# Kernel tuning notes

Measured on AMD Instinct MI355X. Metric: run time of the kernel, lower is better.

Reference implementation:

```python
import jax, jax.numpy as jnp
import numpy as np

HIDDEN = 128
CHNLS = 21
B = 2
T = 15000


def conv1d(x, w, b, stride, pad, groups):
    # x: [N, Cin, L], w: [Cout, Cin/groups, K]
    y = jax.lax.conv_general_dilated(
        x, w, window_strides=(stride,), padding=[(pad, pad)],
        feature_group_count=groups, dimension_numbers=('NCH', 'OIH', 'NCH'))
    return y + b[None, :, None]


def setup_inputs() -> dict:
    key = jax.random.key(0)
    ks = jax.random.split(key, 12)
    d = {}
    d['x'] = jax.random.normal(ks[0], (B, T, CHNLS), dtype=jnp.float32)
    d['ch_vector'] = jax.random.randint(ks[1], (B, CHNLS), 0, CHNLS)
    outs = [HIDDEN // 16 * CHNLS, HIDDEN // 8 * CHNLS, HIDDEN // 4 * CHNLS,
            HIDDEN // 2 * CHNLS, HIDDEN * CHNLS]
    kers = [7, 7, 7, 7, 9]
    for i in range(5):
        d[f'w{i+1}'] = jax.random.normal(ks[2 + i], (outs[i], 1, kers[i]), dtype=jnp.float32) * 0.1
        d[f'b{i+1}'] = jnp.zeros((outs[i],), dtype=jnp.float32)
    d['ch_table'] = jax.random.normal(ks[7], (CHNLS, 512), dtype=jnp.float32) * 0.05
    for i in range(4):
        d[f'mw{i+1}'] = jax.random.normal(ks[8 + i], (1, 1, 4), dtype=jnp.float32) * 0.3
        d[f'mb{i+1}'] = jnp.zeros((1,), dtype=jnp.float32)
    return d


def reference(x, ch_vector, w1, b1, w2, b2, w3, b3, w4, b4, w5, b5,
              ch_table, mw1, mb1, mw2, mb2, mw3, mb3, mw4, mb4):
    # ---- depthwise-style grouped conv stack (groups == in_channels) ----
    h = jnp.transpose(x, (0, 2, 1))                    # [B, CHNLS, T]
    h = conv1d(h, w1, b1, 2, 0, h.shape[1])
    h = conv1d(h, w2, b2, 2, 0, h.shape[1])
    h = conv1d(h, w3, b3, 2, 0, h.shape[1])
    h = conv1d(h, w4, b4, 2, 0, h.shape[1])
    h = conv1d(h, w5, b5, 2, 0, h.shape[1])            # [B, HIDDEN*CHNLS, Tr]

    emb = jnp.transpose(h, (0, 2, 1))                  # [B, Tr, HIDDEN*CHNLS]
    Tr = emb.shape[1]
    emb = emb.reshape(B, Tr, HIDDEN, CHNLS)            # matches torch reshape

    ch_emb = ch_table[ch_vector]                       # [B, CHNLS, 512]
    # torch.einsum('abik, adkj -> abij') with d == 1
    w = jnp.einsum('btik,bkj->btij', emb, ch_emb)      # [B, Tr, HIDDEN, 512]
    w = w.reshape(B, Tr, HIDDEN * 512)

    # ---- per-timestep 1->1 conv stack, batched over B*Tr instead of a loop ----
    z = w.reshape(B * Tr, 1, HIDDEN * 512)
    z = conv1d(z, mw1, mb1, 2, 1, 1)
    z = conv1d(z, mw2, mb2, 2, 1, 1)
    z = jax.nn.gelu(z, approximate=False)
    z = conv1d(z, mw3, mb3, 2, 1, 1)
    z = conv1d(z, mw4, mb4, 2, 1, 1)
    z = jax.nn.gelu(z, approximate=False)              # [B*Tr, 1, HIDDEN*32]
    return z.reshape(B, Tr, HIDDEN * 32)
```

## Files before the change

kernel.cpp:

```cpp
#include <hip/hip_runtime.h>
#include <math.h>


#define NB 2
#define TR 462
#define C5 2688
#define OUTROW 4096

#define T5  42
#define L0T 1531
#define L1T 763
#define L2T 379
#define L3T 187
#define L4T 91
#define SS1 768
#define SS2 384
#define SS3 192
#define SS4 93

__device__ __forceinline__ float gelu_exact(float x) {
    return 0.5f * x * (1.0f + erff(x * 0.7071067811865476f));
}

__device__ __forceinline__ int swz(int a) { return a ^ (((a >> 7) & 7) << 2); }

__device__ __forceinline__ void composite10(const float* A, const float* Bv, float* c) {
#pragma unroll
    for (int r = 0; r < 10; ++r) {
        float acc = 0.f;
#pragma unroll
        for (int p = 0; p < 4; ++p) {
            int q = r - 2 * p;
            if (q >= 0 && q < 4) acc = fmaf(A[p], Bv[q], acc);
        }
        c[r] = acc;
    }
}

__global__ __launch_bounds__(512)
void conv_stack_prep_kernel(const float* __restrict__ x,
                            const float* __restrict__ w1, const float* __restrict__ b1,
                            const float* __restrict__ w2, const float* __restrict__ b2,
                            const float* __restrict__ w3, const float* __restrict__ b3,
                            const float* __restrict__ w4, const float* __restrict__ b4,
                            const float* __restrict__ w5, const float* __restrict__ b5,
                            const float* __restrict__ table, const int* __restrict__ chv,
                            const float* __restrict__ mw1, const float* __restrict__ mw2,
                            float* __restrict__ embT,
                            float* __restrict__ cheCT, float* __restrict__ cheLN4)
{
    const int tile = blockIdx.x;
    const int c    = blockIdx.y;
    const int b    = blockIdx.z;
    const int tid  = threadIdx.x;

    if (tile == 11) {
        if (c != 0 || tid >= 128) return;
        const int m = tid;
        float W1[4], W2[4], c2[10];
#pragma unroll
        for (int q = 0; q < 4; ++q) { W1[q] = mw1[q]; W2[q] = mw2[q]; }
        composite10(W2, W1, c2);
        for (int k = 0; k < 21; ++k) {
            const float* cb = table + (long)chv[b * 21 + k] * 512;
            float acc = 0.f;
            if (m == 0) {
#pragma unroll
                for (int r = 3; r < 10; ++r) acc = fmaf(c2[r], cb[r - 3], acc);
            } else if (m == 127) {
#pragma unroll
                for (int r = 0; r < 7; ++r) acc = fmaf(c2[r], cb[505 + r], acc);
            } else {
                int j0 = 4 * m - 3;
#pragma unroll
                for (int r = 0; r < 10; ++r) acc = fmaf(c2[r], cb[j0 + r], acc);
            }
            cheCT[b * 2688 + m * 21 + k] = acc;
        }
        if (m < 21) {
            const float* cb = table + (long)chv[b * 21 + m] * 512;
            float l = 0.f, n = 0.f;
#pragma unroll
            for (int r = 0; r < 3; ++r)  l = fmaf(c2[r], cb[509 + r], l);
#pragma unroll
            for (int r = 7; r < 10; ++r) n = fmaf(c2[r], cb[r - 7], n);
            cheLN4[b * 84 + m]      = l;
            cheLN4[b * 84 + 21 + m] = n;
            cheLN4[b * 84 + 42 + m] = cb[0];
            cheLN4[b * 84 + 63 + m] = cb[511];
        }
        return;
    }

    __shared__ __align__(16) float A[6144];
    __shared__ __align__(16) float B[6144];
    const int lane = tid & 63;
    const int wq   = tid >> 6;
    const int t0   = tile * T5;

    {
        const float* xp = x + (long)b * 315000L + (long)(32 * t0) * 21L + c;
        for (int i = tid; i < L0T; i += 512) A[i] = xp[(long)i * 21L];
    }
    __syncthreads();

    auto convK7 = [&](const float* SIN, int sstride, bool from_x,
                      float* SOUT, int ostride,
                      const float* wg, const float* bg, int wbase,
                      int nch, int pairs, int Lout, bool b64st) {
        for (int it = 0; it < (nch >> 3); ++it) {
            const int chg = __builtin_amdgcn_readfirstlane((it << 3) + wq);
            const float* wp = wg + (size_t)(wbase + chg) * 7;
            const float W0 = wp[0], Wa = wp[1], Wb = wp[2], Wc = wp[3],
                        Wd = wp[4], We = wp[5], Wf = wp[6];
            const float bb = bg[wbase + chg];
            const float* sin_ch = SIN + (from_x ? 0 : (chg >> 1) * sstride);
            float* sout_ch = SOUT + chg * ostride;
            for (int j = lane; j < pairs; j += 64) {
                const int p = 2 * j;
                const float* s = sin_ch + p * 2;
                const float4 u0 = *(const float4*)(s);
                const float4 u1 = *(const float4*)(s + 4);
                const float4 u2 = *(const float4*)(s + 8);
                float o0 = bb, o1 = bb;
                o0 = fmaf(W0, u0.x, o0); o0 = fmaf(Wa, u0.y, o0); o0 = fmaf(Wb, u0.z, o0);
                o0 = fmaf(Wc, u0.w, o0); o0 = fmaf(Wd, u1.x, o0); o0 = fmaf(We, u1.y, o0);
                o0 = fmaf(Wf, u1.z, o0);
                o1 = fmaf(W0, u0.z, o1); o1 = fmaf(Wa, u0.w, o1); o1 = fmaf(Wb, u1.x, o1);
                o1 = fmaf(Wc, u1.y, o1); o1 = fmaf(Wd, u1.z, o1); o1 = fmaf(We, u1.w, o1);
                o1 = fmaf(Wf, u2.x, o1);
                if (p + 1 < Lout) {
                    if (b64st) *(float2*)(sout_ch + p) = make_float2(o0, o1);
                    else       { sout_ch[p] = o0; sout_ch[p + 1] = o1; }
                } else {
                    sout_ch[p] = o0;
                }
            }
        }
    };

    convK7(A, 0,   true,  B, SS1, w1, b1, 8 * c,  8,  382, L1T, true);
    __syncthreads();
    convK7(B, SS1, false, A, SS2, w2, b2, 16 * c, 16, 190, L2T, true);
    __syncthreads();
    convK7(A, SS2, false, B, SS3, w3, b3, 32 * c, 32, 94,  L3T, true);
    __syncthreads();
    convK7(B, SS3, false, A, SS4, w4, b4, 64 * c, 64, 46,  L4T, false);
    __syncthreads();

    {
        const int ch5 = tid & 127;
        const int th  = tid >> 7;
        const float* wp = w5 + (size_t)(128 * c + ch5) * 9;
        float V[9];
#pragma unroll
        for (int k = 0; k < 9; ++k) V[k] = wp[k];
        const float bb = b5[128 * c + ch5];
        const float* s4ch = A + (ch5 >> 1) * SS4;
        float* obase = embT + ((long)(b * TR + t0)) * C5 + 128 * c + ch5;
#pragma unroll
        for (int iu = 0; iu < 11; ++iu) {
            const int tl = th + 4 * iu;
            if (tl < T5) {
                const float* sp = s4ch + 2 * tl;
                float acc = bb;
#pragma unroll
                for (int k = 0; k < 9; ++k) acc = fmaf(V[k], sp[k], acc);
                obase[(long)tl * C5] = acc;
            }
        }
    }
}

__global__ __launch_bounds__(1024)
void fused_embed_kernel(const float* __restrict__ embT,
                        const float* __restrict__ cheCT,
                        const float* __restrict__ cheLN4,
                        const float* __restrict__ mw1, const float* __restrict__ mb1,
                        const float* __restrict__ mw2, const float* __restrict__ mb2,
                        const float* __restrict__ mw3, const float* __restrict__ mb3,
                        const float* __restrict__ mw4, const float* __restrict__ mb4,
                        float* __restrict__ out)
{
    __shared__ float s_g2[16400];
    __shared__ float s_emb[2688];
    __shared__ float s_ln[84];

    const int t   = blockIdx.x;
    const int b   = blockIdx.y;
    const int tid = threadIdx.x;
    const int i   = tid & 127;
    const int mq  = __builtin_amdgcn_readfirstlane(tid >> 7);

    const float* erow = embT + ((long)(b * TR + t)) * C5;
    if (tid < 672) *(float4*)&s_emb[tid * 4] = ((const float4*)erow)[tid];
    if (tid >= 672 && tid < 756) s_ln[tid - 672] = cheLN4[b * 84 + (tid - 672)];
    if (tid >= 768 && tid < 772)       s_g2[tid - 768] = 0.f;
    else if (tid >= 772 && tid < 788)  s_g2[16380 + (tid - 772) + 4] = 0.f;

    float W1[4], W2[4], W3[4], W4[4];
#pragma unroll
    for (int q = 0; q < 4; ++q) { W1[q] = mw1[q]; W2[q] = mw2[q]; W3[q] = mw3[q]; W4[q] = mw4[q]; }
    const float B1 = mb1[0], B2 = mb2[0], B3 = mb3[0], B4 = mb4[0];
    const float Bc = B2 + B1 * (W2[0] + W2[1] + W2[2] + W2[3]);

    __syncthreads();

    float er[21];
#pragma unroll
    for (int k = 0; k < 21; ++k) er[k] = s_emb[i * 21 + k];

    const float* cp = cheCT + (b * 128 + mq * 16) * 21;
#pragma unroll
    for (int mi4 = 0; mi4 < 4; ++mi4) {
        const int m0 = mq * 16 + mi4 * 4;
        const float* cc = cp + mi4 * 84;
        float z0 = Bc, z1 = Bc, z2 = Bc, z3 = Bc;
#pragma unroll
        for (int k = 0; k < 21; ++k) {
            const float e = er[k];
            z0 = fmaf(e, cc[k],      z0);
            z1 = fmaf(e, cc[21 + k], z1);
            z2 = fmaf(e, cc[42 + k], z2);
            z3 = fmaf(e, cc[63 + k], z3);
        }
        if (mi4 == 0 && mq == 0) {
            float corr = 0.f;
            if (i == 0) {
                float w0 = 0.f;
#pragma unroll
                for (int k = 0; k < 21; ++k) w0 = fmaf(er[k], s_ln[42 + k], w0);
                corr = -W2[0] * (B1 + W1[3] * w0);
            } else {
#pragma unroll
                for (int k = 0; k < 21; ++k) corr = fmaf(s_emb[(i - 1) * 21 + k], s_ln[k], corr);
            }
            z0 += corr;
        }
        if (mi4 == 3 && mq == 7) {
            float corr = 0.f;
            if (i == 127) {
                float wl = 0.f;
#pragma unroll
                for (int k = 0; k < 21; ++k) wl = fmaf(er[k], s_ln[63 + k], wl);
                corr = -W2[3] * (B1 + W1[0] * wl);
            } else {
#pragma unroll
                for (int k = 0; k < 21; ++k) corr = fmaf(s_emb[(i + 1) * 21 + k], s_ln[21 + k], corr);
            }
            z3 += corr;
        }
        float4 q;
        q.x = gelu_exact(z0);
        q.y = gelu_exact(z1);
        q.z = gelu_exact(z2);
        q.w = gelu_exact(z3);
        *(float4*)&s_g2[swz(4 + i * 128 + m0)] = q;
    }
    __syncthreads();

    float c4[10];
    composite10(W4, W3, c4);
    const float Bc2 = B4 + B3 * (W4[0] + W4[1] + W4[2] + W4[3]);
    float* orow = out + ((long)(b * TR + t)) * OUTROW;
#pragma unroll
    for (int s = 0; s < 4; ++s) {
        const int p  = tid + 1024 * s;
        const int a0 = 4 * p;
        const float4 v0 = *(const float4*)&s_g2[swz(a0)];
        const float4 v1 = *(const float4*)&s_g2[swz(a0 + 4)];
        const float4 v2 = *(const float4*)&s_g2[swz(a0 + 8)];
        const float buf[12] = { v0.x, v0.y, v0.z, v0.w,
                                v1.x, v1.y, v1.z, v1.w,
                                v2.x, v2.y, v2.z, v2.w };
        float z = Bc2;
#pragma unroll
        for (int r = 0; r < 10; ++r) z = fmaf(c4[r], buf[r + 1], z);
        if (p == 0)    z -= W4[0] * (B3 + W3[3] * s_g2[swz(4)]);
        if (p == 4095) z -= W4[3] * (B3 + W3[0] * s_g2[swz(16387)]);
        orow[p] = gelu_exact(z);
    }
}

extern "C" void kernel_launch(void* const* d_in, const int* in_sizes, int n_in,
                              void* d_out, int out_size, void* d_ws, size_t ws_size,
                              hipStream_t stream)
{
    const float* x   = (const float*)d_in[0];
    const int*   chv = (const int*)d_in[1];
    const float* w1  = (const float*)d_in[2];  const float* b1 = (const float*)d_in[3];
    const float* w2  = (const float*)d_in[4];  const float* b2 = (const float*)d_in[5];
    const float* w3  = (const float*)d_in[6];  const float* b3 = (const float*)d_in[7];
    const float* w4  = (const float*)d_in[8];  const float* b4 = (const float*)d_in[9];
    const float* w5  = (const float*)d_in[10]; const float* b5 = (const float*)d_in[11];
    const float* tab = (const float*)d_in[12];
    const float* mw1 = (const float*)d_in[13]; const float* mb1 = (const float*)d_in[14];
    const float* mw2 = (const float*)d_in[15]; const float* mb2 = (const float*)d_in[16];
    const float* mw3 = (const float*)d_in[17]; const float* mb3 = (const float*)d_in[18];
    const float* mw4 = (const float*)d_in[19]; const float* mb4 = (const float*)d_in[20];
    float* outp = (float*)d_out;

    float* ws     = (float*)d_ws;
    float* embT   = ws;
    float* cheCT  = ws + 2483712;
    float* cheLN4 = ws + 2489088;

    {
        dim3 grid(12, 21, NB);
        conv_stack_prep_kernel<<<grid, 512, 0, stream>>>(x, w1, b1, w2, b2, w3, b3,
                                                         w4, b4, w5, b5,
                                                         tab, chv, mw1, mw2,
                                                         embT, cheCT, cheLN4);
    }
    {
        dim3 grid(TR, NB);
        fused_embed_kernel<<<grid, 1024, 0, stream>>>(embT, cheCT, cheLN4,
                                                      mw1, mb1, mw2, mb2, mw3, mb3, mw4, mb4,
                                                      outp);
    }
}
```

Measured before the change: 49.44 us.

## Merge conv stack and embed kernels into one cooperative persistent kernel

```diff
diff --git a/kernel.cpp b/kernel.cpp
--- a/kernel.cpp
+++ b/kernel.cpp
@@ -1,11 +1,15 @@
 #include <hip/hip_runtime.h>
+#include <hip/hip_cooperative_groups.h>
 #include <math.h>
+
+namespace cg = cooperative_groups;
 
 
 #define NB 2
 #define TR 462
 #define C5 2688
 #define OUTROW 4096
+#define GRIDB 256
 
 #define T5  42
 #define L0T 1531
@@ -37,248 +41,253 @@
     }
 }
 
-__global__ __launch_bounds__(512)
-void conv_stack_prep_kernel(const float* __restrict__ x,
-                            const float* __restrict__ w1, const float* __restrict__ b1,
-                            const float* __restrict__ w2, const float* __restrict__ b2,
-                            const float* __restrict__ w3, const float* __restrict__ b3,
-                            const float* __restrict__ w4, const float* __restrict__ b4,
-                            const float* __restrict__ w5, const float* __restrict__ b5,
-                            const float* __restrict__ table, const int* __restrict__ chv,
-                            const float* __restrict__ mw1, const float* __restrict__ mw2,
-                            float* __restrict__ embT,
-                            float* __restrict__ cheCT, float* __restrict__ cheLN4)
+__global__ __launch_bounds__(1024, 1)
+void mono_kernel(const float* __restrict__ x,
+                 const float* __restrict__ w1, const float* __restrict__ b1,
+                 const float* __restrict__ w2, const float* __restrict__ b2,
+                 const float* __restrict__ w3, const float* __restrict__ b3,
+                 const float* __restrict__ w4, const float* __restrict__ b4,
+                 const float* __restrict__ w5, const float* __restrict__ b5,
+                 const float* __restrict__ table, const int* __restrict__ chv,
+                 const float* __restrict__ mw1, const float* __restrict__ mb1,
+                 const float* __restrict__ mw2, const float* __restrict__ mb2,
+                 const float* __restrict__ mw3, const float* __restrict__ mb3,
+                 const float* __restrict__ mw4, const float* __restrict__ mb4,
+                 float* __restrict__ embT, float* __restrict__ cheCT,
+                 float* __restrict__ cheLN4, float* __restrict__ out)
 {
-    const int tile = blockIdx.x;
-    const int c    = blockIdx.y;
-    const int b    = blockIdx.z;
-    const int tid  = threadIdx.x;
-
-    if (tile == 11) {
-        if (c != 0 || tid >= 128) return;
-        const int m = tid;
-        float W1[4], W2[4], c2[10];
-#pragma unroll
-        for (int q = 0; q < 4; ++q) { W1[q] = mw1[q]; W2[q] = mw2[q]; }
-        composite10(W2, W1, c2);
-        for (int k = 0; k < 21; ++k) {
-            const float* cb = table + (long)chv[b * 21 + k] * 512;
-            float acc = 0.f;
-            if (m == 0) {
-#pragma unroll
-                for (int r = 3; r < 10; ++r) acc = fmaf(c2[r], cb[r - 3], acc);
-            } else if (m == 127) {
-#pragma unroll
-                for (int r = 0; r < 7; ++r) acc = fmaf(c2[r], cb[505 + r], acc);
-            } else {
-                int j0 = 4 * m - 3;
-#pragma unroll
-                for (int r = 0; r < 10; ++r) acc = fmaf(c2[r], cb[j0 + r], acc);
-            }
-            cheCT[b * 2688 + m * 21 + k] = acc;
-        }
-        if (m < 21) {
-            const float* cb = table + (long)chv[b * 21 + m] * 512;
-            float l = 0.f, n = 0.f;
-#pragma unroll
-            for (int r = 0; r < 3; ++r)  l = fmaf(c2[r], cb[509 + r], l);
-#pragma unroll
-            for (int r = 7; r < 10; ++r) n = fmaf(c2[r], cb[r - 7], n);
-            cheLN4[b * 84 + m]      = l;
-            cheLN4[b * 84 + 21 + m] = n;
-            cheLN4[b * 84 + 42 + m] = cb[0];
-            cheLN4[b * 84 + 63 + m] = cb[511];
-        }
-        return;
-    }
-
-    __shared__ __align__(16) float A[6144];
-    __shared__ __align__(16) float B[6144];
-    const int lane = tid & 63;
-    const int wq   = tid >> 6;
-    const int t0   = tile * T5;
+    __shared__ __align__(16) float smem[24744];
+
+    const int bk  = blockIdx.x;
+    const int tid = threadIdx.x;
 
     {
-        const float* xp = x + (long)b * 315000L + (long)(32 * t0) * 21L + c;
-        for (int i = tid; i < L0T; i += 512) A[i] = xp[(long)i * 21L];
-    }
-    __syncthreads();
-
-    auto convK7 = [&](const float* SIN, int sstride, bool from_x,
-                      float* SOUT, int ostride,
-                      const float* wg, const float* bg, int wbase,
-                      int nch, int pairs, int Lout, bool b64st) {
-        for (int it = 0; it < (nch >> 3); ++it) {
-            const int chg = __builtin_amdgcn_readfirstlane((it << 3) + wq);
-            const float* wp = wg + (size_t)(wbase + chg) * 7;
-            const float W0 = wp[0], Wa = wp[1], Wb = wp[2], Wc = wp[3],
-                        Wd = wp[4], We = wp[5], Wf = wp[6];
-            const float bb = bg[wbase + chg];
-            const float* sin_ch = SIN + (from_x ? 0 : (chg >> 1) * sstride);
-            float* sout_ch = SOUT + chg * ostride;
-            for (int j = lane; j < pairs; j += 64) {
-                const int p = 2 * j;
-                const float* s = sin_ch + p * 2;
-                const float4 u0 = *(const float4*)(s);
-                const float4 u1 = *(const float4*)(s + 4);
-                const float4 u2 = *(const float4*)(s + 8);
-                float o0 = bb, o1 = bb;
-                o0 = fmaf(W0, u0.x, o0); o0 = fmaf(Wa, u0.y, o0); o0 = fmaf(Wb, u0.z, o0);
-                o0 = fmaf(Wc, u0.w, o0); o0 = fmaf(Wd, u1.x, o0); o0 = fmaf(We, u1.y, o0);
-                o0 = fmaf(Wf, u1.z, o0);
-                o1 = fmaf(W0, u0.z, o1); o1 = fmaf(Wa, u0.w, o1); o1 = fmaf(Wb, u1.x, o1);
-                o1 = fmaf(Wc, u1.y, o1); o1 = fmaf(Wd, u1.z, o1); o1 = fmaf(We, u1.w, o1);
-                o1 = fmaf(Wf, u2.x, o1);
-                if (p + 1 < Lout) {
-                    if (b64st) *(float2*)(sout_ch + p) = make_float2(o0, o1);
-                    else       { sout_ch[p] = o0; sout_ch[p + 1] = o1; }
+        const int h   = tid >> 9;
+        const int tl  = tid & 511;
+        const int job = 2 * bk + h;
+        if (job < 462) {
+            const int tile = job % 11;
+            const int c    = (job / 11) % 21;
+            const int b    = job / 231;
+            float* A = smem + h * 12288;
+            float* B = A + 6144;
+            const int lane = tl & 63;
+            const int wq   = tl >> 6;
+            const int t0   = tile * T5;
+
+            const float* xp = x + (long)b * 315000L + (long)(32 * t0) * 21L + c;
+            for (int i2 = tl; i2 < L0T; i2 += 512) A[i2] = xp[(long)i2 * 21L];
+            __syncthreads();
+
+            auto convK7 = [&](const float* SIN, int sstride, bool from_x,
+                              float* SOUT, int ostride,
+                              const float* wg, const float* bg, int wbase,
+                              int nch, int pairs, int Lout, bool b64st) {
+                for (int it = 0; it < (nch >> 3); ++it) {
+                    const int chg = __builtin_amdgcn_readfirstlane((it << 3) + wq);
+                    const float* wp = wg + (size_t)(wbase + chg) * 7;
+                    const float W0 = wp[0], Wa = wp[1], Wb = wp[2], Wc = wp[3],
+                                Wd = wp[4], We = wp[5], Wf = wp[6];
+                    const float bb = bg[wbase + chg];
+                    const float* sin_ch = SIN + (from_x ? 0 : (chg >> 1) * sstride);
+                    float* sout_ch = SOUT + chg * ostride;
+                    for (int j = lane; j < pairs; j += 64) {
+                        const int p = 2 * j;
+                        const float* s = sin_ch + p * 2;
+                        const float4 u0 = *(const float4*)(s);
+                        const float4 u1 = *(const float4*)(s + 4);
+                        const float4 u2 = *(const float4*)(s + 8);
+                        float o0 = bb, o1 = bb;
+                        o0 = fmaf(W0, u0.x, o0); o0 = fmaf(Wa, u0.y, o0); o0 = fmaf(Wb, u0.z, o0);
+                        o0 = fmaf(Wc, u0.w, o0); o0 = fmaf(Wd, u1.x, o0); o0 = fmaf(We, u1.y, o0);
+                        o0 = fmaf(Wf, u1.z, o0);
+                        o1 = fmaf(W0, u0.z, o1); o1 = fmaf(Wa, u0.w, o1); o1 = fmaf(Wb, u1.x, o1);
+                        o1 = fmaf(Wc, u1.y, o1); o1 = fmaf(Wd, u1.z, o1); o1 = fmaf(We, u1.w, o1);
+                        o1 = fmaf(Wf, u2.x, o1);
+                        if (p + 1 < Lout) {
+                            if (b64st) *(float2*)(sout_ch + p) = make_float2(o0, o1);
+                            else       { sout_ch[p] = o0; sout_ch[p + 1] = o1; }
+                        } else {
+                            sout_ch[p] = o0;
+                        }
+                    }
+                }
+            };
+
+            convK7(A, 0,   true,  B, SS1, w1, b1, 8 * c,  8,  382, L1T, true);
+            __syncthreads();
+            convK7(B, SS1, false, A, SS2, w2, b2, 16 * c, 16, 190, L2T, true);
+            __syncthreads();
+            convK7(A, SS2, false, B, SS3, w3, b3, 32 * c, 32, 94,  L3T, true);
+            __syncthreads();
+            convK7(B, SS3, false, A, SS4, w4, b4, 64 * c, 64, 46,  L4T, false);
+            __syncthreads();
+
+            {
+                const int ch5 = tl & 127;
+                const int th  = (tl >> 7) & 3;
+                const float* wp = w5 + (size_t)(128 * c + ch5) * 9;
+                float V[9];
+#pragma unroll
+                for (int k = 0; k < 9; ++k) V[k] = wp[k];
+                const float bb = b5[128 * c + ch5];
+                const float* s4ch = A + (ch5 >> 1) * SS4;
+                float* obase = embT + ((long)(b * TR + t0)) * C5 + 128 * c + ch5;
+#pragma unroll
+                for (int iu = 0; iu < 11; ++iu) {
+                    const int tl5 = th + 4 * iu;
+                    if (tl5 < T5) {
+                        const float* sp = s4ch + 2 * tl5;
+                        float acc = bb;
+#pragma unroll
+                        for (int k = 0; k < 9; ++k) acc = fmaf(V[k], sp[k], acc);
+                        obase[(long)tl5 * C5] = acc;
+                    }
+                }
+            }
+        } else if (job < 464 && tl < 128) {
+            const int b = job - 462;
+            const int m = tl;
+            float W1[4], W2[4], c2[10];
+#pragma unroll
+            for (int q = 0; q < 4; ++q) { W1[q] = mw1[q]; W2[q] = mw2[q]; }
+            composite10(W2, W1, c2);
+            for (int k = 0; k < 21; ++k) {
+                const float* cb = table + (long)chv[b * 21 + k] * 512;
+                float acc = 0.f;
+                if (m == 0) {
+#pragma unroll
+                    for (int r = 3; r < 10; ++r) acc = fmaf(c2[r], cb[r - 3], acc);
+                } else if (m == 127) {
+#pragma unroll
+                    for (int r = 0; r < 7; ++r) acc = fmaf(c2[r], cb[505 + r], acc);
                 } else {
-                    sout_ch[p] = o0;
-                }
-            }
-        }
-    };
-
-    convK7(A, 0,   true,  B, SS1, w1, b1, 8 * c,  8,  382, L1T, true);
-    __syncthreads();
-    convK7(B, SS1, false, A, SS2, w2, b2, 16 * c, 16, 190, L2T, true);
-    __syncthreads();
-    convK7(A, SS2, false, B, SS3, w3, b3, 32 * c, 32, 94,  L3T, true);
-    __syncthreads();
-    convK7(B, SS3, false, A, SS4, w4, b4, 64 * c, 64, 46,  L4T, false);
-    __syncthreads();
-
-    {
-        const int ch5 = tid & 127;
-        const int th  = tid >> 7;
-        const float* wp = w5 + (size_t)(128 * c + ch5) * 9;
-        float V[9];
-#pragma unroll
-        for (int k = 0; k < 9; ++k) V[k] = wp[k];
-        const float bb = b5[128 * c + ch5];
-        const float* s4ch = A + (ch5 >> 1) * SS4;
-        float* obase = embT + ((long)(b * TR + t0)) * C5 + 128 * c + ch5;
-#pragma unroll
-        for (int iu = 0; iu < 11; ++iu) {
-            const int tl = th + 4 * iu;
-            if (tl < T5) {
-                const float* sp = s4ch + 2 * tl;
-                float acc = bb;
-#pragma unroll
-                for (int k = 0; k < 9; ++k) acc = fmaf(V[k], sp[k], acc);
-                obase[(long)tl * C5] = acc;
+                    int j0 = 4 * m - 3;
+#pragma unroll
+                    for (int r = 0; r < 10; ++r) acc = fmaf(c2[r], cb[j0 + r], acc);
+                }
+                cheCT[b * 2688 + m * 21 + k] = acc;
+            }
+            if (m < 21) {
+                const float* cb = table + (long)chv[b * 21 + m] * 512;
+                float l = 0.f, n = 0.f;
+#pragma unroll
+                for (int r = 0; r < 3; ++r)  l = fmaf(c2[r], cb[509 + r], l);
+#pragma unroll
+                for (int r = 7; r < 10; ++r) n = fmaf(c2[r], cb[r - 7], n);
+                cheLN4[b * 84 + m]      = l;
+                cheLN4[b * 84 + 21 + m] = n;
+                cheLN4[b * 84 + 42 + m] = cb[0];
+                cheLN4[b * 84 + 63 + m] = cb[511];
             }
         }
     }
-}
-
-__global__ __launch_bounds__(1024)
-void fused_embed_kernel(const float* __restrict__ embT,
-                        const float* __restrict__ cheCT,
-                        const float* __restrict__ cheLN4,
-                        const float* __restrict__ mw1, const float* __restrict__ mb1,
-                        const float* __restrict__ mw2, const float* __restrict__ mb2,
-                        const float* __restrict__ mw3, const float* __restrict__ mb3,
-                        const float* __restrict__ mw4, const float* __restrict__ mb4,
-                        float* __restrict__ out)
-{
-    __shared__ float s_g2[16400];
-    __shared__ float s_emb[2688];
-    __shared__ float s_ln[84];
-
-    const int t   = blockIdx.x;
-    const int b   = blockIdx.y;
-    const int tid = threadIdx.x;
-    const int i   = tid & 127;
-    const int mq  = __builtin_amdgcn_readfirstlane(tid >> 7);
-
-    const float* erow = embT + ((long)(b * TR + t)) * C5;
-    if (tid < 672) *(float4*)&s_emb[tid * 4] = ((const float4*)erow)[tid];
-    if (tid >= 672 && tid < 756) s_ln[tid - 672] = cheLN4[b * 84 + (tid - 672)];
-    if (tid >= 768 && tid < 772)       s_g2[tid - 768] = 0.f;
-    else if (tid >= 772 && tid < 788)  s_g2[16380 + (tid - 772) + 4] = 0.f;
+
+    cg::this_grid().sync();
+
+    float* s_g2  = smem;
+    float* s_emb = smem + 16400;
+    float* s_ln  = smem + 24576;
+
+    if (tid < 168) s_ln[tid] = cheLN4[tid];
+    if (tid >= 256 && tid < 260) s_g2[tid - 256] = 0.f;
+    if (tid >= 260 && tid < 276) s_g2[16384 + (tid - 260)] = 0.f;
 
     float W1[4], W2[4], W3[4], W4[4];
 #pragma unroll
     for (int q = 0; q < 4; ++q) { W1[q] = mw1[q]; W2[q] = mw2[q]; W3[q] = mw3[q]; W4[q] = mw4[q]; }
     const float B1 = mb1[0], B2 = mb2[0], B3 = mb3[0], B4 = mb4[0];
     const float Bc = B2 + B1 * (W2[0] + W2[1] + W2[2] + W2[3]);
-
-    __syncthreads();
-
-    float er[21];
-#pragma unroll
-    for (int k = 0; k < 21; ++k) er[k] = s_emb[i * 21 + k];
-
-    const float* cp = cheCT + (b * 128 + mq * 16) * 21;
-#pragma unroll
-    for (int mi4 = 0; mi4 < 4; ++mi4) {
-        const int m0 = mq * 16 + mi4 * 4;
-        const float* cc = cp + mi4 * 84;
-        float z0 = Bc, z1 = Bc, z2 = Bc, z3 = Bc;
-#pragma unroll
-        for (int k = 0; k < 21; ++k) {
-            const float e = er[k];
-            z0 = fmaf(e, cc[k],      z0);
-            z1 = fmaf(e, cc[21 + k], z1);
-            z2 = fmaf(e, cc[42 + k], z2);
-            z3 = fmaf(e, cc[63 + k], z3);
-        }
-        if (mi4 == 0 && mq == 0) {
-            float corr = 0.f;
-            if (i == 0) {
-                float w0 = 0.f;
-#pragma unroll
-                for (int k = 0; k < 21; ++k) w0 = fmaf(er[k], s_ln[42 + k], w0);
-                corr = -W2[0] * (B1 + W1[3] * w0);
-            } else {
-#pragma unroll
-                for (int k = 0; k < 21; ++k) corr = fmaf(s_emb[(i - 1) * 21 + k], s_ln[k], corr);
-            }
-            z0 += corr;
-        }
-        if (mi4 == 3 && mq == 7) {
-            float corr = 0.f;
-            if (i == 127) {
-                float wl = 0.f;
-#pragma unroll
-                for (int k = 0; k < 21; ++k) wl = fmaf(er[k], s_ln[63 + k], wl);
-                corr = -W2[3] * (B1 + W1[0] * wl);
-            } else {
-#pragma unroll
-                for (int k = 0; k < 21; ++k) corr = fmaf(s_emb[(i + 1) * 21 + k], s_ln[21 + k], corr);
-            }
-            z3 += corr;
-        }
-        float4 q;
-        q.x = gelu_exact(z0);
-        q.y = gelu_exact(z1);
-        q.z = gelu_exact(z2);
-        q.w = gelu_exact(z3);
-        *(float4*)&s_g2[swz(4 + i * 128 + m0)] = q;
-    }
-    __syncthreads();
-
     float c4[10];
     composite10(W4, W3, c4);
     const float Bc2 = B4 + B3 * (W4[0] + W4[1] + W4[2] + W4[3]);
-    float* orow = out + ((long)(b * TR + t)) * OUTROW;
-#pragma unroll
-    for (int s = 0; s < 4; ++s) {
-        const int p  = tid + 1024 * s;
-        const int a0 = 4 * p;
-        const float4 v0 = *(const float4*)&s_g2[swz(a0)];
-        const float4 v1 = *(const float4*)&s_g2[swz(a0 + 4)];
-        const float4 v2 = *(const float4*)&s_g2[swz(a0 + 8)];
-        const float buf[12] = { v0.x, v0.y, v0.z, v0.w,
-                                v1.x, v1.y, v1.z, v1.w,
-                                v2.x, v2.y, v2.z, v2.w };
-        float z = Bc2;
-#pragma unroll
-        for (int r = 0; r < 10; ++r) z = fmaf(c4[r], buf[r + 1], z);
-        if (p == 0)    z -= W4[0] * (B3 + W3[3] * s_g2[swz(4)]);
-        if (p == 4095) z -= W4[3] * (B3 + W3[0] * s_g2[swz(16387)]);
-        orow[p] = gelu_exact(z);
+
+    const int i  = tid & 127;
+    const int mq = __builtin_amdgcn_readfirstlane(tid >> 7);
+
+    for (int r = 0; r < 4; ++r) {
+        const int job = bk + 256 * r;
+        if (job < NB * TR) {
+            const int t = job % TR;
+            const int b = job / TR;
+            const float* lnb = s_ln + b * 84;
+
+            const float* erow = embT + ((long)(b * TR + t)) * C5;
+            if (tid < 672) *(float4*)&s_emb[tid * 4] = ((const float4*)erow)[tid];
+            __syncthreads();
+
+            float er[21];
+#pragma unroll
+            for (int k = 0; k < 21; ++k) er[k] = s_emb[i * 21 + k];
+
+            const float* cp = cheCT + (b * 128 + mq * 16) * 21;
+#pragma unroll
+            for (int mi4 = 0; mi4 < 4; ++mi4) {
+                const int m0 = mq * 16 + mi4 * 4;
+                const float* cc = cp + mi4 * 84;
+                float z0 = Bc, z1 = Bc, z2 = Bc, z3 = Bc;
+#pragma unroll
+                for (int k = 0; k < 21; ++k) {
+                    const float e = er[k];
+                    z0 = fmaf(e, cc[k],      z0);
+                    z1 = fmaf(e, cc[21 + k], z1);
+                    z2 = fmaf(e, cc[42 + k], z2);
+                    z3 = fmaf(e, cc[63 + k], z3);
+                }
+                if (mi4 == 0 && mq == 0) {
+                    float corr = 0.f;
+                    if (i == 0) {
+                        float w0 = 0.f;
+#pragma unroll
+                        for (int k = 0; k < 21; ++k) w0 = fmaf(er[k], lnb[42 + k], w0);
+                        corr = -W2[0] * (B1 + W1[3] * w0);
+                    } else {
+#pragma unroll
+                        for (int k = 0; k < 21; ++k) corr = fmaf(s_emb[(i - 1) * 21 + k], lnb[k], corr);
+                    }
+                    z0 += corr;
+                }
+                if (mi4 == 3 && mq == 7) {
+                    float corr = 0.f;
+                    if (i == 127) {
+                        float wl = 0.f;
+#pragma unroll
+                        for (int k = 0; k < 21; ++k) wl = fmaf(er[k], lnb[63 + k], wl);
+                        corr = -W2[3] * (B1 + W1[0] * wl);
+                    } else {
+#pragma unroll
+                        for (int k = 0; k < 21; ++k) corr = fmaf(s_emb[(i + 1) * 21 + k], lnb[21 + k], corr);
+                    }
+                    z3 += corr;
+                }
+                float4 q;
+                q.x = gelu_exact(z0);
+                q.y = gelu_exact(z1);
+                q.z = gelu_exact(z2);
+                q.w = gelu_exact(z3);
+                *(float4*)&s_g2[swz(4 + i * 128 + m0)] = q;
+            }
+            __syncthreads();
+
+            float* orow = out + ((long)(b * TR + t)) * OUTROW;
+#pragma unroll
+            for (int s = 0; s < 4; ++s) {
+                const int p  = tid + 1024 * s;
+                const int a0 = 4 * p;
+                const float4 v0 = *(const float4*)&s_g2[swz(a0)];
+                const float4 v1 = *(const float4*)&s_g2[swz(a0 + 4)];
+                const float4 v2 = *(const float4*)&s_g2[swz(a0 + 8)];
+                const float buf[12] = { v0.x, v0.y, v0.z, v0.w,
+                                        v1.x, v1.y, v1.z, v1.w,
+                                        v2.x, v2.y, v2.z, v2.w };
+                float z = Bc2;
+#pragma unroll
+                for (int rr = 0; rr < 10; ++rr) z = fmaf(c4[rr], buf[rr + 1], z);
+                if (p == 0)    z -= W4[0] * (B3 + W3[3] * s_g2[swz(4)]);
+                if (p == 4095) z -= W4[3] * (B3 + W3[0] * s_g2[swz(16387)]);
+                orow[p] = gelu_exact(z);
+            }
+        }
     }
 }
 
@@ -305,17 +314,17 @@
     float* cheCT  = ws + 2483712;
     float* cheLN4 = ws + 2489088;
 
-    {
-        dim3 grid(12, 21, NB);
-        conv_stack_prep_kernel<<<grid, 512, 0, stream>>>(x, w1, b1, w2, b2, w3, b3,
-                                                         w4, b4, w5, b5,
-                                                         tab, chv, mw1, mw2,
-                                                         embT, cheCT, cheLN4);
-    }
-    {
-        dim3 grid(TR, NB);
-        fused_embed_kernel<<<grid, 1024, 0, stream>>>(embT, cheCT, cheLN4,
-                                                      mw1, mb1, mw2, mb2, mw3, mb3, mw4, mb4,
-                                                      outp);
-    }
+    void* args[] = {
+        (void*)&x,
+        (void*)&w1, (void*)&b1, (void*)&w2, (void*)&b2, (void*)&w3, (void*)&b3,
+        (void*)&w4, (void*)&b4, (void*)&w5, (void*)&b5,
+        (void*)&tab, (void*)&chv,
+        (void*)&mw1, (void*)&mb1, (void*)&mw2, (void*)&mb2,
+        (void*)&mw3, (void*)&mb3, (void*)&mw4, (void*)&mb4,
+        (void*)&embT, (void*)&cheCT, (void*)&cheLN4, (void*)&outp
+    };
+
+    hipLaunchCooperativeKernel((const void*)mono_kernel,
+                               dim3(GRIDB), dim3(1024),
+                               args, 0, stream);
 }
```

After: 140.2 us. 184% more time.
